# Performance work log

Measured on AMD Instinct MI355X. Metric: run time of the kernel, lower is better.

The kernel has to match this reference:

```python
import jax, jax.numpy as jnp
import numpy as np

N_NODES = 50000


def gcn_conv(x, src, dst, W, b):
    """PyG GCNConv: y = D^-1/2 (A + I) D^-1/2 (x W) + b, deg counted with self-loops."""
    n = x.shape[0]
    xw = x @ W                                             # [N, out]
    # degree with self-loops (in-degree at dst, +1 for the self-loop)
    deg = jnp.zeros((n,), x.dtype).at[dst].add(1.0) + 1.0  # [N]
    dinv = deg ** -0.5
    coef = dinv[src] * dinv[dst]                           # [E]
    msgs = xw[src] * coef[:, None]                         # [E, out]  (irregular gather)
    agg = jax.ops.segment_sum(msgs, dst, num_segments=n)   # scatter-add
    agg = agg + xw * (dinv * dinv)[:, None]                # self-loop contribution
    return agg + b


def setup_inputs() -> dict:
    key = jax.random.key(0)
    ks = jax.random.split(key, 10)
    d_in, h1, h2, n_cls, e_cls = 64, 256, 128, 2, 2
    x = jax.random.normal(ks[0], (N_NODES, d_in), dtype=jnp.float32)
    edge_index = jax.random.randint(ks[1], (2, 800000), 0, N_NODES, dtype=jnp.int64)

    def glorot(k, shape):
        lim = float(np.sqrt(6.0 / (shape[0] + shape[1])))
        return jax.random.uniform(k, shape, jnp.float32, -lim, lim)

    return {
        "x": x,
        "edge_index": edge_index,
        "W1": glorot(ks[2], (d_in, h1)), "b1": jnp.zeros((h1,), jnp.float32),
        "W2": glorot(ks[3], (h1, h2)), "b2": jnp.zeros((h2,), jnp.float32),
        "node_W": glorot(ks[4], (h2, n_cls)), "node_b": jnp.zeros((n_cls,), jnp.float32),
        "edge_W": glorot(ks[5], (2 * h2, e_cls)), "edge_b": jnp.zeros((e_cls,), jnp.float32),
    }


def reference(x, edge_index, W1, b1, W2, b2, node_W, node_b, edge_W, edge_b):
    src, dst = edge_index[0], edge_index[1]
    h = gcn_conv(x, src, dst, W1, b1)
    h = jax.nn.relu(h)
    embeddings = gcn_conv(h, src, dst, W2, b2)   # last layer: no relu; kept as embeddings
    # dropout is identity in eval mode
    node_x = embeddings @ node_W + node_b        # [N, node_classes]
    edge_feat = jnp.concatenate([embeddings[src], embeddings[dst]], axis=-1)  # [E, 2*h2]
    edge_x = edge_feat @ edge_W + edge_b         # [E, edge_classes]
    return node_x, edge_x
```

## Files before the change

kernel.cpp:

```cpp
#include <hip/hip_runtime.h>

static constexpr int DIN = 64;
static constexpr int H1  = 256;
static constexpr int H2  = 128;

using half8 = _Float16 __attribute__((ext_vector_type(8)));
using f32x4 = float __attribute__((ext_vector_type(4)));

__device__ __forceinline__ unsigned short f2h_bits(float f) {
  _Float16 h = (_Float16)f;
  unsigned short u;
  __builtin_memcpy(&u, &h, 2);
  return u;
}
__device__ __forceinline__ float h_bits2f(unsigned u) {
  unsigned short us = (unsigned short)(u & 0xffffu);
  _Float16 h;
  __builtin_memcpy(&h, &us, 2);
  return (float)h;
}

__global__ __launch_bounds__(256) void
k_prep(int* __restrict__ hist, int N,
       const float* __restrict__ x, _Float16* __restrict__ xh, int nvec8,
       const float* __restrict__ W1, _Float16* __restrict__ Wf1,
       const float* __restrict__ W2, const float* __restrict__ nW,
       const float* __restrict__ nb, const float* __restrict__ eW,
       const float* __restrict__ b2, float* __restrict__ Wz8,
       float* __restrict__ consts,
       int NB0, int NB1, int NB2) {
  const int b = blockIdx.x;
  const int t = threadIdx.x;
  if (b < NB0) {
    int i = b * 256 + t;
    if (i < N) hist[i] = 0;
  } else if (b < NB1) {
    int i = (b - NB0) * 256 + t;
    if (i < nvec8) {
      const float4* x4 = (const float4*)x;
      float4 a = x4[i * 2 + 0];
      float4 bb = x4[i * 2 + 1];
      half8 h;
      h[0] = (_Float16)a.x; h[1] = (_Float16)a.y; h[2] = (_Float16)a.z; h[3] = (_Float16)a.w;
      h[4] = (_Float16)bb.x; h[5] = (_Float16)bb.y; h[6] = (_Float16)bb.z; h[7] = (_Float16)bb.w;
      *(half8*)(xh + (size_t)i * 8) = h;
    }
  } else if (b < NB2) {
    int i = (b - NB1) * 256 + t;
    if (i < DIN * H1) {
      int j    = i & 7;
      int lane = (i >> 3) & 63;
      int rest = i >> 9;
      int tt   = rest % (DIN / 32);
      int c    = rest / (DIN / 32);
      int k    = tt * 32 + (lane >> 4) * 8 + j;
      int col  = c * 16 + (lane & 15);
      Wf1[i] = (_Float16)W1[k * H1 + col];
    }
  } else {
    int k = t;
    float acc[6] = {0, 0, 0, 0, 0, 0};
    for (int m = 0; m < H2; ++m) {
      float w = W2[k * H2 + m];
      acc[0] = fmaf(w, nW[m * 2 + 0], acc[0]);
      acc[1] = fmaf(w, nW[m * 2 + 1], acc[1]);
      acc[2] = fmaf(w, eW[m * 2 + 0], acc[2]);
      acc[3] = fmaf(w, eW[m * 2 + 1], acc[3]);
      acc[4] = fmaf(w, eW[(H2 + m) * 2 + 0], acc[4]);
      acc[5] = fmaf(w, eW[(H2 + m) * 2 + 1], acc[5]);
    }
#pragma unroll
    for (int c = 0; c < 6; ++c) Wz8[k * 8 + c] = acc[c];
    Wz8[k * 8 + 6] = 0.0f; Wz8[k * 8 + 7] = 0.0f;
    if (k == 0) {
      float c0 = nb[0], c1 = nb[1], c2 = 0, c3 = 0, c4 = 0, c5 = 0;
      for (int m = 0; m < H2; ++m) {
        float bv = b2[m];
        c0 = fmaf(bv, nW[m * 2 + 0], c0);
        c1 = fmaf(bv, nW[m * 2 + 1], c1);
        c2 = fmaf(bv, eW[m * 2 + 0], c2);
        c3 = fmaf(bv, eW[m * 2 + 1], c3);
        c4 = fmaf(bv, eW[(H2 + m) * 2 + 0], c4);
        c5 = fmaf(bv, eW[(H2 + m) * 2 + 1], c5);
      }
      consts[0] = c0; consts[1] = c1; consts[2] = c2;
      consts[3] = c3; consts[4] = c4; consts[5] = c5;
      consts[6] = 0.0f; consts[7] = 0.0f;
    }
  }
}

__global__ void k_hist(const int* __restrict__ dst, int* __restrict__ hist,
                       unsigned short* __restrict__ rank, int E) {
  int i = blockIdx.x * blockDim.x + threadIdx.x;
  int e = i * 4;
  if (e + 3 < E) {
    int4 d4 = *(const int4*)(dst + e);
    int r0 = atomicAdd(&hist[d4.x], 1);
    int r1 = atomicAdd(&hist[d4.y], 1);
    int r2 = atomicAdd(&hist[d4.z], 1);
    int r3 = atomicAdd(&hist[d4.w], 1);
    unsigned pk0 = (unsigned)(r0 & 0xffff) | ((unsigned)(r1 & 0xffff) << 16);
    unsigned pk1 = (unsigned)(r2 & 0xffff) | ((unsigned)(r3 & 0xffff) << 16);
    *(unsigned*)(rank + e)     = pk0;
    *(unsigned*)(rank + e + 2) = pk1;
  } else {
    for (; e < E; ++e) {
      int r = atomicAdd(&hist[dst[e]], 1);
      rank[e] = (unsigned short)r;
    }
  }
}

__global__ void k_scan1(const int* __restrict__ hist, int* __restrict__ offs,
                        int* __restrict__ bsum, float* __restrict__ dinv, int N) {
  __shared__ int ws[4];
  const int t = threadIdx.x;
  const int base = blockIdx.x * 1024 + t * 4;
  int4 v = make_int4(0, 0, 0, 0);
  if (base + 3 < N) v = *(const int4*)(hist + base);
  else {
    if (base + 0 < N) v.x = hist[base + 0];
    if (base + 1 < N) v.y = hist[base + 1];
    if (base + 2 < N) v.z = hist[base + 2];
    if (base + 3 < N) v.w = hist[base + 3];
  }
  if (base + 3 < N) {
    float4 dv = make_float4(rsqrtf((float)v.x + 1.0f), rsqrtf((float)v.y + 1.0f),
                            rsqrtf((float)v.z + 1.0f), rsqrtf((float)v.w + 1.0f));
    *(float4*)(dinv + base) = dv;
  } else {
    if (base + 0 < N) dinv[base + 0] = rsqrtf((float)v.x + 1.0f);
    if (base + 1 < N) dinv[base + 1] = rsqrtf((float)v.y + 1.0f);
    if (base + 2 < N) dinv[base + 2] = rsqrtf((float)v.z + 1.0f);
    if (base + 3 < N) dinv[base + 3] = rsqrtf((float)v.w + 1.0f);
  }
  int tsum = v.x + v.y + v.z + v.w;
  int lane = t & 63, wid = t >> 6;
  int incl = tsum;
#pragma unroll
  for (int off = 1; off < 64; off <<= 1) {
    int u = __shfl_up(incl, off);
    if (lane >= off) incl += u;
  }
  if (lane == 63) ws[wid] = incl;
  __syncthreads();
  int wbase = 0;
  for (int w = 0; w < wid; ++w) wbase += ws[w];
  int excl = wbase + incl - tsum;
  int4 o;
  o.x = excl;
  o.y = excl + v.x;
  o.z = excl + v.x + v.y;
  o.w = excl + v.x + v.y + v.z;
  if (base + 3 < N) *(int4*)(offs + base) = o;
  else {
    if (base + 0 < N) offs[base + 0] = o.x;
    if (base + 1 < N) offs[base + 1] = o.y;
    if (base + 2 < N) offs[base + 2] = o.z;
    if (base + 3 < N) offs[base + 3] = o.w;
  }
  if (t == 255) bsum[blockIdx.x] = wbase + incl;
}

__global__ void k_scan2(const int* __restrict__ bsum, int* __restrict__ bbase,
                        int* __restrict__ offs, int nb, int N) {
  int t = threadIdx.x;
  int v = (t < nb) ? bsum[t] : 0;
  int incl = v;
#pragma unroll
  for (int off = 1; off < 64; off <<= 1) {
    int u = __shfl_up(incl, off);
    if (t >= off) incl += u;
  }
  if (t < 64) bbase[t] = incl - v;
  if (t == nb - 1) offs[N] = v;
}

__global__ void k_build(const int* __restrict__ src, const int* __restrict__ dst,
                        const unsigned short* __restrict__ rank,
                        const int* __restrict__ offs, const int* __restrict__ bbase,
                        const float* __restrict__ dinv,
                        unsigned* __restrict__ csr, int E) {
  int i = blockIdx.x * blockDim.x + threadIdx.x;
  int e = i * 4;
  if (e + 3 < E) {
    int4 s4 = *(const int4*)(src + e);
    int4 d4 = *(const int4*)(dst + e);
    unsigned rr0 = *(const unsigned*)(rank + e);
    unsigned rr1 = *(const unsigned*)(rank + e + 2);
    int pos0 = offs[d4.x] + bbase[d4.x >> 10] + (int)(rr0 & 0xffffu);
    int pos1 = offs[d4.y] + bbase[d4.y >> 10] + (int)(rr0 >> 16);
    int pos2 = offs[d4.z] + bbase[d4.z >> 10] + (int)(rr1 & 0xffffu);
    int pos3 = offs[d4.w] + bbase[d4.w >> 10] + (int)(rr1 >> 16);
    unsigned v0 = ((unsigned)s4.x << 16) | f2h_bits(dinv[s4.x]);
    unsigned v1 = ((unsigned)s4.y << 16) | f2h_bits(dinv[s4.y]);
    unsigned v2 = ((unsigned)s4.z << 16) | f2h_bits(dinv[s4.z]);
    unsigned v3 = ((unsigned)s4.w << 16) | f2h_bits(dinv[s4.w]);
    csr[pos0] = v0;
    csr[pos1] = v1;
    csr[pos2] = v2;
    csr[pos3] = v3;
  } else {
    for (; e < E; ++e) {
      int s = src[e], d = dst[e];
      int pos = offs[d] + bbase[d >> 10] + (int)rank[e];
      csr[pos] = ((unsigned)s << 16) | f2h_bits(dinv[s]);
    }
  }
}

__global__ __launch_bounds__(256) void
k_gather64(const int* __restrict__ offs, const int* __restrict__ bbase,
           const unsigned* __restrict__ csr, const float* __restrict__ dinv,
           const _Float16* __restrict__ xw, _Float16* __restrict__ out, int N) {
  constexpr int C = 64;
  int wave = (int)((blockIdx.x * (size_t)blockDim.x + threadIdx.x) >> 6);
  int lane = threadIdx.x & 63;
  int half = lane >> 5;
  int node = wave * 2 + half;
  if (node >= N) return;
  int l32   = lane & 31;
  int group = l32 >> 3;
  int sub   = l32 & 7;
  int ch0   = sub * 8;
  int hb    = half << 5;
  float dv = dinv[node];
  int j0 = offs[node] + bbase[node >> 10];
  int j1 = offs[node + 1] + bbase[(node + 1) >> 10];

  float acc[8];
  if (group == 0) {
    half8 v = *(const half8*)(xw + (size_t)node * C + ch0);
    float sc = dv * dv;
#pragma unroll
    for (int k = 0; k < 8; ++k) acc[k] = (float)v[k] * sc;
  } else {
#pragma unroll
    for (int k = 0; k < 8; ++k) acc[k] = 0.0f;
  }

  for (int base = j0; base < j1; base += 32) {
    int myj = base + l32;
    unsigned u_l = 0;
    if (myj < j1) u_l = csr[myj];
    int cnt = min(32, j1 - base);
    for (int k = 0; k < cnt; k += 8) {
      unsigned ua = (unsigned)__shfl((int)u_l, hb + k + group);
      unsigned ub = (unsigned)__shfl((int)u_l, hb + k + 4 + group);
      half8 va, vb;
      bool ba = (ua != 0), bb = (ub != 0);
      if (ba) va = *(const half8*)(xw + (size_t)(ua >> 16) * C + ch0);
      if (bb) vb = *(const half8*)(xw + (size_t)(ub >> 16) * C + ch0);
      if (ba) {
        float c = h_bits2f(ua) * dv;
#pragma unroll
        for (int k2 = 0; k2 < 8; ++k2) acc[k2] = fmaf((float)va[k2], c, acc[k2]);
      }
      if (bb) {
        float c = h_bits2f(ub) * dv;
#pragma unroll
        for (int k2 = 0; k2 < 8; ++k2) acc[k2] = fmaf((float)vb[k2], c, acc[k2]);
      }
    }
  }

#pragma unroll
  for (int off = 8; off < 32; off <<= 1) {
#pragma unroll
    for (int k = 0; k < 8; ++k) acc[k] += __shfl_xor(acc[k], off);
  }

  if (group == 0) {
    half8 o;
#pragma unroll
    for (int k = 0; k < 8; ++k) o[k] = (_Float16)acc[k];
    *(half8*)(out + (size_t)node * C + ch0) = o;
  }
}

__global__ __launch_bounds__(256) void
k_mgemm_z(const _Float16* __restrict__ A, const _Float16* __restrict__ Wf,
          const float* __restrict__ bias, const float* __restrict__ Wz8,
          float* __restrict__ z, int M) {
  constexpr int K = DIN, NOUT = H1;
  constexpr int NC = NOUT / 16;
  constexpr int NT = K / 32;
  const int wave = threadIdx.x >> 6;
  const int lane = threadIdx.x & 63;
  const int rowbase = blockIdx.x * 128 + wave * 32;
  if (rowbase >= M) return;
  const int r  = lane & 15;
  const int kb = lane >> 4;
  int row0 = rowbase + r;       if (row0 >= M) row0 = M - 1;
  int row1 = rowbase + 16 + r;  if (row1 >= M) row1 = M - 1;
  const _Float16* a0p = A + (size_t)row0 * K + kb * 8;
  const _Float16* a1p = A + (size_t)row1 * K + kb * 8;

  f32x4 acc[2][NC];
#pragma unroll
  for (int rb = 0; rb < 2; ++rb)
#pragma unroll
    for (int c = 0; c < NC; ++c) acc[rb][c] = (f32x4)0.0f;

#pragma unroll
  for (int t = 0; t < NT; ++t) {
    half8 a0 = *(const half8*)(a0p + t * 32);
    half8 a1 = *(const half8*)(a1p + t * 32);
#pragma unroll
    for (int c = 0; c < NC; ++c) {
      half8 bf = ((const half8*)Wf)[(size_t)(c * NT + t) * 64 + lane];
      acc[0][c] = __builtin_amdgcn_mfma_f32_16x16x32_f16(a0, bf, acc[0][c], 0, 0, 0);
      acc[1][c] = __builtin_amdgcn_mfma_f32_16x16x32_f16(a1, bf, acc[1][c], 0, 0, 0);
    }
  }

  float zc[2][4][6];
#pragma unroll
  for (int rb = 0; rb < 2; ++rb)
#pragma unroll
    for (int j = 0; j < 4; ++j)
#pragma unroll
      for (int ch = 0; ch < 6; ++ch) zc[rb][j][ch] = 0.0f;

#pragma unroll
  for (int c = 0; c < NC; ++c) {
    int col = c * 16 + r;
    const float* wp = Wz8 + col * 8;
    float4 w0 = *(const float4*)wp;
    float2 w1 = *(const float2*)(wp + 4);
    float bv = bias[col];
#pragma unroll
    for (int rb = 0; rb < 2; ++rb) {
#pragma unroll
      for (int j = 0; j < 4; ++j) {
        float hv = fmaxf(acc[rb][c][j] + bv, 0.0f);
        zc[rb][j][0] = fmaf(hv, w0.x, zc[rb][j][0]);
        zc[rb][j][1] = fmaf(hv, w0.y, zc[rb][j][1]);
        zc[rb][j][2] = fmaf(hv, w0.z, zc[rb][j][2]);
        zc[rb][j][3] = fmaf(hv, w0.w, zc[rb][j][3]);
        zc[rb][j][4] = fmaf(hv, w1.x, zc[rb][j][4]);
        zc[rb][j][5] = fmaf(hv, w1.y, zc[rb][j][5]);
      }
    }
  }

#pragma unroll
  for (int off = 1; off < 16; off <<= 1) {
#pragma unroll
    for (int rb = 0; rb < 2; ++rb)
#pragma unroll
      for (int j = 0; j < 4; ++j)
#pragma unroll
        for (int ch = 0; ch < 6; ++ch)
          zc[rb][j][ch] += __shfl_xor(zc[rb][j][ch], off);
  }

  if (r == 0) {
#pragma unroll
    for (int rb = 0; rb < 2; ++rb) {
      int growbase = rowbase + rb * 16 + kb * 4;
#pragma unroll
      for (int j = 0; j < 4; ++j) {
        int grow = growbase + j;
        if (grow < M) {
          float4 lo = make_float4(zc[rb][j][0], zc[rb][j][1], zc[rb][j][2], zc[rb][j][3]);
          float4 hi = make_float4(zc[rb][j][4], zc[rb][j][5], 0.0f, 0.0f);
          *(float4*)(z + (size_t)grow * 8)     = lo;
          *(float4*)(z + (size_t)grow * 8 + 4) = hi;
        }
      }
    }
  }
}

__global__ __launch_bounds__(256) void
k_gatherz(const int* __restrict__ offs, const int* __restrict__ bbase,
          const unsigned* __restrict__ csr, const float* __restrict__ dinv,
          const float* __restrict__ z, const float* __restrict__ consts,
          float* __restrict__ node_out, float* __restrict__ p, float* __restrict__ q,
          int N) {
  int wave = (int)((blockIdx.x * (size_t)blockDim.x + threadIdx.x) >> 6);
  int lane = threadIdx.x & 63;
  int quad = lane >> 4;
  int node = wave * 4 + quad;
  if (node >= N) return;
  int l16   = lane & 15;
  int group = l16 >> 1;
  int sub   = l16 & 1;
  int hb    = quad << 4;
  float dv = dinv[node];
  int j0 = offs[node] + bbase[node >> 10];
  int j1 = offs[node + 1] + bbase[(node + 1) >> 10];

  float4 acc = make_float4(0.0f, 0.0f, 0.0f, 0.0f);
  if (group == 0) {
    float4 v = *(const float4*)(z + (size_t)node * 8 + sub * 4);
    float sc = dv * dv;
    acc = make_float4(v.x * sc, v.y * sc, v.z * sc, v.w * sc);
  }

  for (int base = j0; base < j1; base += 16) {
    int myj = base + l16;
    unsigned u_l = 0;
    if (myj < j1) u_l = csr[myj];
    int cnt = min(16, j1 - base);
    for (int k = 0; k < cnt; k += 8) {
      unsigned u = (unsigned)__shfl((int)u_l, hb + k + group);
      if (u != 0) {
        int   s = (int)(u >> 16);
        float c = h_bits2f(u) * dv;
        float4 v = *(const float4*)(z + (size_t)s * 8 + sub * 4);
        acc.x = fmaf(v.x, c, acc.x);
        acc.y = fmaf(v.y, c, acc.y);
        acc.z = fmaf(v.z, c, acc.z);
        acc.w = fmaf(v.w, c, acc.w);
      }
    }
  }

#pragma unroll
  for (int off = 2; off < 16; off <<= 1) {
    acc.x += __shfl_xor(acc.x, off);
    acc.y += __shfl_xor(acc.y, off);
    acc.z += __shfl_xor(acc.z, off);
    acc.w += __shfl_xor(acc.w, off);
  }

  if (l16 == 0) {
    float2 no = make_float2(acc.x + consts[0], acc.y + consts[1]);
    float2 pp = make_float2(acc.z + consts[2], acc.w + consts[3]);
    *(float2*)(node_out + (size_t)node * 2) = no;
    *(float2*)(p + (size_t)node * 2) = pp;
  } else if (l16 == 1) {
    float2 qq = make_float2(acc.x + consts[4], acc.y + consts[5]);
    *(float2*)(q + (size_t)node * 2) = qq;
  }
}

__global__ void k_edge(const int* __restrict__ src, const int* __restrict__ dst,
                       const float* __restrict__ p, const float* __restrict__ q,
                       const float* __restrict__ eb, float* __restrict__ eout, int E) {
  int i = blockIdx.x * blockDim.x + threadIdx.x;
  int e = i * 4;
  float e0 = eb[0], e1 = eb[1];
  if (e + 3 < E) {
    int4 s4 = *(const int4*)(src + e);
    int4 d4 = *(const int4*)(dst + e);
    float2 P0 = *(const float2*)(p + (size_t)s4.x * 2);
    float2 Q0 = *(const float2*)(q + (size_t)d4.x * 2);
    float2 P1 = *(const float2*)(p + (size_t)s4.y * 2);
    float2 Q1 = *(const float2*)(q + (size_t)d4.y * 2);
    float2 P2 = *(const float2*)(p + (size_t)s4.z * 2);
    float2 Q2 = *(const float2*)(q + (size_t)d4.z * 2);
    float2 P3 = *(const float2*)(p + (size_t)s4.w * 2);
    float2 Q3 = *(const float2*)(q + (size_t)d4.w * 2);
    float4 oa, ob;
    oa.x = P0.x + Q0.x + e0;  oa.y = P0.y + Q0.y + e1;
    oa.z = P1.x + Q1.x + e0;  oa.w = P1.y + Q1.y + e1;
    ob.x = P2.x + Q2.x + e0;  ob.y = P2.y + Q2.y + e1;
    ob.z = P3.x + Q3.x + e0;  ob.w = P3.y + Q3.y + e1;
    *(float4*)(eout + (size_t)e * 2)     = oa;
    *(float4*)(eout + (size_t)e * 2 + 4) = ob;
  } else {
    for (; e < E; ++e) {
      int s = src[e], d = dst[e];
      float2 P = *(const float2*)(p + (size_t)s * 2);
      float2 Q = *(const float2*)(q + (size_t)d * 2);
      float2 o;
      o.x = P.x + Q.x + e0;
      o.y = P.y + Q.y + e1;
      *(float2*)(eout + (size_t)e * 2) = o;
    }
  }
}

extern "C" void kernel_launch(void* const* d_in, const int* in_sizes, int n_in,
                              void* d_out, int out_size, void* d_ws, size_t ws_size,
                              hipStream_t stream) {
  const float* x   = (const float*)d_in[0];
  const int*   ei  = (const int*)d_in[1];
  const float* W1  = (const float*)d_in[2];
  const float* b1  = (const float*)d_in[3];
  const float* W2  = (const float*)d_in[4];
  const float* b2  = (const float*)d_in[5];
  const float* nW  = (const float*)d_in[6];
  const float* nb  = (const float*)d_in[7];
  const float* eW  = (const float*)d_in[8];
  const float* eb  = (const float*)d_in[9];

  const int N = in_sizes[0] / DIN;
  const int E = in_sizes[1] / 2;
  const int* src = ei;
  const int* dst = ei + E;

  float* fws   = (float*)d_ws;
  float* dinv  = fws;
  float* p     = dinv + N;
  float* q     = p + 2 * (size_t)N;
  float* z     = q + 2 * (size_t)N;
  float* Wz8   = z + 8 * (size_t)N;
  float* consts = Wz8 + 2048;
  _Float16* xh    = (_Float16*)(consts + 8);
  _Float16* aggxh = xh + (size_t)DIN * N;
  _Float16* Wf1   = aggxh + (size_t)DIN * N;
  int* hist = (int*)(Wf1 + DIN * H1);
  int* offs = hist + N;
  int* bsum = offs + N + 1;
  int* bbase = bsum + 64;
  unsigned short* rank = (unsigned short*)(bbase + 64);
  unsigned* csr = (unsigned*)(rank + E);

  float* node_out = (float*)d_out;
  float* edge_out = (float*)d_out + 2 * (size_t)N;

  const int nb_blk = (N + 1023) / 1024;
  const int nvec8  = N * DIN / 8;

  const int NB0 = (N + 255) / 256;
  const int NB1 = NB0 + (nvec8 + 255) / 256;
  const int NB2 = NB1 + (DIN * H1 + 255) / 256;
  const int NBP = NB2 + 1;

  k_prep<<<NBP, 256, 0, stream>>>(hist, N, x, xh, nvec8, W1, Wf1,
                                  W2, nW, nb, eW, b2, Wz8, consts, NB0, NB1, NB2);
  k_hist<<<((E + 3) / 4 + 255) / 256, 256, 0, stream>>>(dst, hist, rank, E);
  k_scan1<<<nb_blk, 256, 0, stream>>>(hist, offs, bsum, dinv, N);
  k_scan2<<<1, 64, 0, stream>>>(bsum, bbase, offs, nb_blk, N);
  k_build<<<((E + 3) / 4 + 255) / 256, 256, 0, stream>>>(src, dst, rank, offs, bbase, dinv, csr, E);

  {
    int waves = (N + 1) / 2;
    k_gather64<<<(waves + 3) / 4, 256, 0, stream>>>(offs, bbase, csr, dinv, xh, aggxh, N);
  }
  k_mgemm_z<<<(N + 127) / 128, 256, 0, stream>>>(aggxh, Wf1, b1, Wz8, z, N);

  {
    int waves = (N + 3) / 4;
    k_gatherz<<<(waves + 3) / 4, 256, 0, stream>>>(offs, bbase, csr, dinv, z, consts, node_out, p, q, N);
  }

  k_edge<<<((E + 3) / 4 + 255) / 256, 256, 0, stream>>>(src, dst, p, q, eb, edge_out, E);
}
```

Before: 129.7 us.

## Fuse block-sum scan into scan1, unroll gathers, transpose MFMA epilogue in z-GEMM

Several changes land together. The second scan kernel is folded into the first using a last-block-done atomic counter, which removes one launch. The gather loops in both aggregation kernels are unrolled to issue four or two independent row loads per step, giving more memory-level parallelism. The MFMA operands in the z GEMM are swapped so each lane holds a column slice, which lets the bias and Wz8 epilogue reduce across lane groups with fewer shuffles and fewer z stores. The added risk is the correctness of the fence and atomic pattern, and higher register pressure from the unrolled loops.

```diff
diff --git a/kernel.cpp b/kernel.cpp
--- a/kernel.cpp
+++ b/kernel.cpp
@@ -27,13 +27,14 @@
        const float* __restrict__ W2, const float* __restrict__ nW,
        const float* __restrict__ nb, const float* __restrict__ eW,
        const float* __restrict__ b2, float* __restrict__ Wz8,
-       float* __restrict__ consts,
+       float* __restrict__ consts, int* __restrict__ done,
        int NB0, int NB1, int NB2) {
   const int b = blockIdx.x;
   const int t = threadIdx.x;
   if (b < NB0) {
     int i = b * 256 + t;
     if (i < N) hist[i] = 0;
+    if (b == 0 && t == 0) *done = 0;
   } else if (b < NB1) {
     int i = (b - NB0) * 256 + t;
     if (i < nvec8) {
@@ -113,8 +114,10 @@
 }
 
 __global__ void k_scan1(const int* __restrict__ hist, int* __restrict__ offs,
-                        int* __restrict__ bsum, float* __restrict__ dinv, int N) {
+                        int* __restrict__ bsum, float* __restrict__ dinv,
+                        int* __restrict__ bbase, int* __restrict__ done, int N) {
   __shared__ int ws[4];
+  __shared__ int amLast;
   const int t = threadIdx.x;
   const int base = blockIdx.x * 1024 + t * 4;
   int4 v = make_int4(0, 0, 0, 0);
@@ -160,21 +163,24 @@
     if (base + 2 < N) offs[base + 2] = o.z;
     if (base + 3 < N) offs[base + 3] = o.w;
   }
-  if (t == 255) bsum[blockIdx.x] = wbase + incl;
-}
-
-__global__ void k_scan2(const int* __restrict__ bsum, int* __restrict__ bbase,
-                        int* __restrict__ offs, int nb, int N) {
-  int t = threadIdx.x;
-  int v = (t < nb) ? bsum[t] : 0;
-  int incl = v;
-#pragma unroll
-  for (int off = 1; off < 64; off <<= 1) {
-    int u = __shfl_up(incl, off);
-    if (t >= off) incl += u;
-  }
-  if (t < 64) bbase[t] = incl - v;
-  if (t == nb - 1) offs[N] = v;
+  if (t == 255) {
+    bsum[blockIdx.x] = wbase + incl;
+    __threadfence();
+    amLast = (atomicAdd(done, 1) == (int)gridDim.x - 1) ? 1 : 0;
+  }
+  __syncthreads();
+  if (amLast && t < 64) {
+    int nb = (int)gridDim.x;
+    int bv = (t < nb) ? atomicAdd(&bsum[t], 0) : 0;
+    int bincl = bv;
+#pragma unroll
+    for (int off = 1; off < 64; off <<= 1) {
+      int u = __shfl_up(bincl, off);
+      if (t >= off) bincl += u;
+    }
+    bbase[t] = bincl - bv;
+    if (t == nb - 1) offs[N] = bv;
+  }
 }
 
 __global__ void k_build(const int* __restrict__ src, const int* __restrict__ dst,
@@ -242,25 +248,38 @@
 
   for (int base = j0; base < j1; base += 32) {
     int myj = base + l32;
-    unsigned u_l = 0;
-    if (myj < j1) u_l = csr[myj];
+    unsigned u_l = (myj < j1) ? csr[myj] : 0u;
     int cnt = min(32, j1 - base);
-    for (int k = 0; k < cnt; k += 8) {
-      unsigned ua = (unsigned)__shfl((int)u_l, hb + k + group);
-      unsigned ub = (unsigned)__shfl((int)u_l, hb + k + 4 + group);
-      half8 va, vb;
-      bool ba = (ua != 0), bb = (ub != 0);
-      if (ba) va = *(const half8*)(xw + (size_t)(ua >> 16) * C + ch0);
-      if (bb) vb = *(const half8*)(xw + (size_t)(ub >> 16) * C + ch0);
-      if (ba) {
-        float c = h_bits2f(ua) * dv;
-#pragma unroll
-        for (int k2 = 0; k2 < 8; ++k2) acc[k2] = fmaf((float)va[k2], c, acc[k2]);
-      }
-      if (bb) {
-        float c = h_bits2f(ub) * dv;
-#pragma unroll
-        for (int k2 = 0; k2 < 8; ++k2) acc[k2] = fmaf((float)vb[k2], c, acc[k2]);
+    for (int k = 0; k < cnt; k += 16) {
+      unsigned u0 = (unsigned)__shfl((int)u_l, hb + k + group);
+      unsigned u1 = (unsigned)__shfl((int)u_l, hb + k + 4 + group);
+      unsigned u2 = (unsigned)__shfl((int)u_l, hb + k + 8 + group);
+      unsigned u3 = (unsigned)__shfl((int)u_l, hb + k + 12 + group);
+      half8 v0, v1, v2, v3;
+      bool b0 = u0 != 0, b1 = u1 != 0, b2 = u2 != 0, b3 = u3 != 0;
+      if (b0) v0 = *(const half8*)(xw + (size_t)(u0 >> 16) * C + ch0);
+      if (b1) v1 = *(const half8*)(xw + (size_t)(u1 >> 16) * C + ch0);
+      if (b2) v2 = *(const half8*)(xw + (size_t)(u2 >> 16) * C + ch0);
+      if (b3) v3 = *(const half8*)(xw + (size_t)(u3 >> 16) * C + ch0);
+      if (b0) {
+        float c = h_bits2f(u0) * dv;
+#pragma unroll
+        for (int k2 = 0; k2 < 8; ++k2) acc[k2] = fmaf((float)v0[k2], c, acc[k2]);
+      }
+      if (b1) {
+        float c = h_bits2f(u1) * dv;
+#pragma unroll
+        for (int k2 = 0; k2 < 8; ++k2) acc[k2] = fmaf((float)v1[k2], c, acc[k2]);
+      }
+      if (b2) {
+        float c = h_bits2f(u2) * dv;
+#pragma unroll
+        for (int k2 = 0; k2 < 8; ++k2) acc[k2] = fmaf((float)v2[k2], c, acc[k2]);
+      }
+      if (b3) {
+        float c = h_bits2f(u3) * dv;
+#pragma unroll
+        for (int k2 = 0; k2 < 8; ++k2) acc[k2] = fmaf((float)v3[k2], c, acc[k2]);
       }
     }
   }
@@ -299,9 +318,9 @@
 
   f32x4 acc[2][NC];
 #pragma unroll
-  for (int rb = 0; rb < 2; ++rb)
-#pragma unroll
-    for (int c = 0; c < NC; ++c) acc[rb][c] = (f32x4)0.0f;
+  for (int g = 0; g < 2; ++g)
+#pragma unroll
+    for (int c = 0; c < NC; ++c) acc[g][c] = (f32x4)0.0f;
 
 #pragma unroll
   for (int t = 0; t < NT; ++t) {
@@ -310,65 +329,61 @@
 #pragma unroll
     for (int c = 0; c < NC; ++c) {
       half8 bf = ((const half8*)Wf)[(size_t)(c * NT + t) * 64 + lane];
-      acc[0][c] = __builtin_amdgcn_mfma_f32_16x16x32_f16(a0, bf, acc[0][c], 0, 0, 0);
-      acc[1][c] = __builtin_amdgcn_mfma_f32_16x16x32_f16(a1, bf, acc[1][c], 0, 0, 0);
-    }
-  }
-
-  float zc[2][4][6];
-#pragma unroll
-  for (int rb = 0; rb < 2; ++rb)
-#pragma unroll
-    for (int j = 0; j < 4; ++j)
-#pragma unroll
-      for (int ch = 0; ch < 6; ++ch) zc[rb][j][ch] = 0.0f;
+      acc[0][c] = __builtin_amdgcn_mfma_f32_16x16x32_f16(bf, a0, acc[0][c], 0, 0, 0);
+      acc[1][c] = __builtin_amdgcn_mfma_f32_16x16x32_f16(bf, a1, acc[1][c], 0, 0, 0);
+    }
+  }
+
+  float zc[2][6];
+#pragma unroll
+  for (int g = 0; g < 2; ++g)
+#pragma unroll
+    for (int ch = 0; ch < 6; ++ch) zc[g][ch] = 0.0f;
 
 #pragma unroll
   for (int c = 0; c < NC; ++c) {
-    int col = c * 16 + r;
-    const float* wp = Wz8 + col * 8;
-    float4 w0 = *(const float4*)wp;
-    float2 w1 = *(const float2*)(wp + 4);
-    float bv = bias[col];
-#pragma unroll
-    for (int rb = 0; rb < 2; ++rb) {
-#pragma unroll
-      for (int j = 0; j < 4; ++j) {
-        float hv = fmaxf(acc[rb][c][j] + bv, 0.0f);
-        zc[rb][j][0] = fmaf(hv, w0.x, zc[rb][j][0]);
-        zc[rb][j][1] = fmaf(hv, w0.y, zc[rb][j][1]);
-        zc[rb][j][2] = fmaf(hv, w0.z, zc[rb][j][2]);
-        zc[rb][j][3] = fmaf(hv, w0.w, zc[rb][j][3]);
-        zc[rb][j][4] = fmaf(hv, w1.x, zc[rb][j][4]);
-        zc[rb][j][5] = fmaf(hv, w1.y, zc[rb][j][5]);
-      }
-    }
-  }
-
-#pragma unroll
-  for (int off = 1; off < 16; off <<= 1) {
-#pragma unroll
-    for (int rb = 0; rb < 2; ++rb)
-#pragma unroll
-      for (int j = 0; j < 4; ++j)
-#pragma unroll
-        for (int ch = 0; ch < 6; ++ch)
-          zc[rb][j][ch] += __shfl_xor(zc[rb][j][ch], off);
-  }
-
-  if (r == 0) {
-#pragma unroll
-    for (int rb = 0; rb < 2; ++rb) {
-      int growbase = rowbase + rb * 16 + kb * 4;
-#pragma unroll
-      for (int j = 0; j < 4; ++j) {
-        int grow = growbase + j;
-        if (grow < M) {
-          float4 lo = make_float4(zc[rb][j][0], zc[rb][j][1], zc[rb][j][2], zc[rb][j][3]);
-          float4 hi = make_float4(zc[rb][j][4], zc[rb][j][5], 0.0f, 0.0f);
-          *(float4*)(z + (size_t)grow * 8)     = lo;
-          *(float4*)(z + (size_t)grow * 8 + 4) = hi;
-        }
+    float4 b4 = *(const float4*)(bias + c * 16 + kb * 4);
+    float bj[4] = {b4.x, b4.y, b4.z, b4.w};
+#pragma unroll
+    for (int j = 0; j < 4; ++j) {
+      const float* wp = Wz8 + (c * 16 + kb * 4 + j) * 8;
+      float4 w0 = *(const float4*)wp;
+      float2 w1 = *(const float2*)(wp + 4);
+      float hv0 = fmaxf(acc[0][c][j] + bj[j], 0.0f);
+      float hv1 = fmaxf(acc[1][c][j] + bj[j], 0.0f);
+      zc[0][0] = fmaf(hv0, w0.x, zc[0][0]);
+      zc[0][1] = fmaf(hv0, w0.y, zc[0][1]);
+      zc[0][2] = fmaf(hv0, w0.z, zc[0][2]);
+      zc[0][3] = fmaf(hv0, w0.w, zc[0][3]);
+      zc[0][4] = fmaf(hv0, w1.x, zc[0][4]);
+      zc[0][5] = fmaf(hv0, w1.y, zc[0][5]);
+      zc[1][0] = fmaf(hv1, w0.x, zc[1][0]);
+      zc[1][1] = fmaf(hv1, w0.y, zc[1][1]);
+      zc[1][2] = fmaf(hv1, w0.z, zc[1][2]);
+      zc[1][3] = fmaf(hv1, w0.w, zc[1][3]);
+      zc[1][4] = fmaf(hv1, w1.x, zc[1][4]);
+      zc[1][5] = fmaf(hv1, w1.y, zc[1][5]);
+    }
+  }
+
+#pragma unroll
+  for (int off = 16; off < 64; off <<= 1) {
+#pragma unroll
+    for (int g = 0; g < 2; ++g)
+#pragma unroll
+      for (int ch = 0; ch < 6; ++ch)
+        zc[g][ch] += __shfl_xor(zc[g][ch], off);
+  }
+
+  if (lane < 16) {
+#pragma unroll
+    for (int g = 0; g < 2; ++g) {
+      int grow = rowbase + g * 16 + r;
+      if (grow < M) {
+        float4 lo = make_float4(zc[g][0], zc[g][1], zc[g][2], zc[g][3]);
+        float4 hi = make_float4(zc[g][4], zc[g][5], 0.0f, 0.0f);
+        *(float4*)(z + (size_t)grow * 8)     = lo;
+        *(float4*)(z + (size_t)grow * 8 + 4) = hi;
       }
     }
   }
@@ -402,19 +417,28 @@
 
   for (int base = j0; base < j1; base += 16) {
     int myj = base + l16;
-    unsigned u_l = 0;
-    if (myj < j1) u_l = csr[myj];
+    unsigned u_l = (myj < j1) ? csr[myj] : 0u;
     int cnt = min(16, j1 - base);
-    for (int k = 0; k < cnt; k += 8) {
-      unsigned u = (unsigned)__shfl((int)u_l, hb + k + group);
-      if (u != 0) {
-        int   s = (int)(u >> 16);
-        float c = h_bits2f(u) * dv;
-        float4 v = *(const float4*)(z + (size_t)s * 8 + sub * 4);
-        acc.x = fmaf(v.x, c, acc.x);
-        acc.y = fmaf(v.y, c, acc.y);
-        acc.z = fmaf(v.z, c, acc.z);
-        acc.w = fmaf(v.w, c, acc.w);
+    for (int k = 0; k < cnt; k += 16) {
+      unsigned u0 = (unsigned)__shfl((int)u_l, hb + k + group);
+      unsigned u1 = (unsigned)__shfl((int)u_l, hb + k + 8 + group);
+      float4 v0, v1;
+      bool b0 = u0 != 0, b1 = u1 != 0;
+      if (b0) v0 = *(const float4*)(z + (size_t)(u0 >> 16) * 8 + sub * 4);
+      if (b1) v1 = *(const float4*)(z + (size_t)(u1 >> 16) * 8 + sub * 4);
+      if (b0) {
+        float c = h_bits2f(u0) * dv;
+        acc.x = fmaf(v0.x, c, acc.x);
+        acc.y = fmaf(v0.y, c, acc.y);
+        acc.z = fmaf(v0.z, c, acc.z);
+        acc.w = fmaf(v0.w, c, acc.w);
+      }
+      if (b1) {
+        float c = h_bits2f(u1) * dv;
+        acc.x = fmaf(v1.x, c, acc.x);
+        acc.y = fmaf(v1.y, c, acc.y);
+        acc.z = fmaf(v1.z, c, acc.z);
+        acc.w = fmaf(v1.w, c, acc.w);
       }
     }
   }
@@ -508,7 +532,8 @@
   int* offs = hist + N;
   int* bsum = offs + N + 1;
   int* bbase = bsum + 64;
-  unsigned short* rank = (unsigned short*)(bbase + 64);
+  int* done  = bbase + 64;
+  unsigned short* rank = (unsigned short*)(done + 64);
   unsigned* csr = (unsigned*)(rank + E);
 
   float* node_out = (float*)d_out;
@@ -523,10 +548,9 @@
   const int NBP = NB2 + 1;
 
   k_prep<<<NBP, 256, 0, stream>>>(hist, N, x, xh, nvec8, W1, Wf1,
-                                  W2, nW, nb, eW, b2, Wz8, consts, NB0, NB1, NB2);
+                                  W2, nW, nb, eW, b2, Wz8, consts, done, NB0, NB1, NB2);
   k_hist<<<((E + 3) / 4 + 255) / 256, 256, 0, stream>>>(dst, hist, rank, E);
-  k_scan1<<<nb_blk, 256, 0, stream>>>(hist, offs, bsum, dinv, N);
-  k_scan2<<<1, 64, 0, stream>>>(bsum, bbase, offs, nb_blk, N);
+  k_scan1<<<nb_blk, 256, 0, stream>>>(hist, offs, bsum, dinv, bbase, done, N);
   k_build<<<((E + 3) / 4 + 255) / 256, 256, 0, stream>>>(src, dst, rank, offs, bbase, dinv, csr, E);
 
   {
```

New measurement: 128.7 us. No clear change (-0.7%).
